# Kernel tuning notes

Hardware: AMD Instinct MI355X
Metric: run time of the kernel (lower is better)

Reference implementation:

```python
import jax, jax.numpy as jnp
import numpy as np

EMBED_DIM = 1024
HEADS = 16
D_HEAD = EMBED_DIM // HEADS
B, S = 2, 2048


def setup_inputs() -> dict:
    key = jax.random.key(0)
    ks = jax.random.split(key, 7)
    scale = 1.0 / np.sqrt(EMBED_DIM)
    inp = {
        "key": jax.random.normal(ks[0], (B, S, EMBED_DIM), dtype=jnp.float32),
        "query": jax.random.normal(ks[1], (B, S, EMBED_DIM), dtype=jnp.float32),
        "value": jax.random.normal(ks[2], (B, S, EMBED_DIM), dtype=jnp.float32),
        # causal mask, broadcastable to [B, H, Sq, Sk]
        "mask": jnp.tril(jnp.ones((S, S), dtype=bool))[None, None, :, :],
        # torch nn.Linear weights: [out_features, in_features], applied as x @ W.T
        "Wq": jax.random.normal(ks[3], (EMBED_DIM, EMBED_DIM), dtype=jnp.float32) * scale,
        "Wk": jax.random.normal(ks[4], (EMBED_DIM, EMBED_DIM), dtype=jnp.float32) * scale,
        "Wv": jax.random.normal(ks[5], (EMBED_DIM, EMBED_DIM), dtype=jnp.float32) * scale,
        "Wo": jax.random.normal(ks[6], (EMBED_DIM, EMBED_DIM), dtype=jnp.float32) * scale,
    }
    return inp


def reference(key, query, value, mask, Wq, Wk, Wv, Wo):
    b, sq, _ = query.shape
    sk = key.shape[1]
    # projections (torch Linear: x @ W.T), reshape to [B, H, S, Dh]
    q = (query @ Wq.T).reshape(b, sq, HEADS, D_HEAD).transpose(0, 2, 1, 3)
    k = (key @ Wk.T).reshape(b, sk, HEADS, D_HEAD).transpose(0, 2, 1, 3)
    v = (value @ Wv.T).reshape(b, sk, HEADS, D_HEAD).transpose(0, 2, 1, 3)
    # scaled dot-product scores [B, H, Sq, Sk]
    scores = jnp.einsum("bhqd,bhkd->bhqk", q, k) / jnp.sqrt(jnp.float32(D_HEAD))
    scores = jnp.where(mask, scores, jnp.float32(-1e9))
    attn = jax.nn.softmax(scores, axis=-1)
    # dropout p=0.0 -> identity
    out = jnp.einsum("bhqk,bhkd->bhqd", attn, v)  # [B, H, Sq, Dh]
    out = out.transpose(0, 2, 1, 3).reshape(b, sq, EMBED_DIM)
    return out @ Wo.T
```

## Files before the change

kernel.cpp:

```cpp
#include <hip/hip_runtime.h>
#include <stdint.h>


typedef unsigned short ushort_t;
typedef __attribute__((ext_vector_type(8))) __bf16 bf16x8;
typedef __attribute__((ext_vector_type(4))) float floatx4;

#define EMBED 1024
#define SEQ   2048
#define NH    16
#define DH    64
#define QK_SCALE 0.18033688011112042f

__device__ inline ushort_t f2b(float x) {
  unsigned u = __float_as_uint(x);
  u += 0x7FFFu + ((u >> 16) & 1u);
  return (ushort_t)(u >> 16);
}

__device__ inline unsigned pk2(float a, float b) {
  unsigned ua = __float_as_uint(a) + 0x8000u;
  unsigned ub = __float_as_uint(b) + 0x8000u;
  return __builtin_amdgcn_perm(ub, ua, 0x07060302u);
}

__device__ inline void gl_lds16(const ushort_t* g, ushort_t* l) {
  __builtin_amdgcn_global_load_lds(
      (const __attribute__((address_space(1))) unsigned int*)g,
      (__attribute__((address_space(3))) unsigned int*)l, 16, 0, 0);
}

struct CvtArgs {
  const float* src[16];
  ushort_t*    dst[16];
  float        scale[16];
};

__global__ __launch_bounds__(256) void cvt_kernel(CvtArgs a) {
  const int chunk = blockIdx.x >> 9;
  const int off = ((blockIdx.x & 511) << 11) + (threadIdx.x << 3);
  const float sc = a.scale[chunk];
  const float4* s = (const float4*)(a.src[chunk] + off);
  float4 f0 = s[0], f1 = s[1];
  union { ushort_t u[8]; uint4 v; } o;
  o.u[0] = f2b(f0.x * sc); o.u[1] = f2b(f0.y * sc);
  o.u[2] = f2b(f0.z * sc); o.u[3] = f2b(f0.w * sc);
  o.u[4] = f2b(f1.x * sc); o.u[5] = f2b(f1.y * sc);
  o.u[6] = f2b(f1.z * sc); o.u[7] = f2b(f1.w * sc);
  *(uint4*)(a.dst[chunk] + off) = o.v;
}

template <int NSUB>
__device__ inline void gemm_core(const ushort_t* __restrict__ A,
                                 const ushort_t* __restrict__ W,
                                 char* __restrict__ Cv, const int mode,
                                 const int K, const int ldc,
                                 const int m0, const int n0) {
  __shared__ ushort_t As[16 * 512];
  __shared__ ushort_t Bs[NSUB * 4 * 512];
  const int tid  = threadIdx.x;
  const int lane = tid & 63;
  const int wid  = tid >> 6;
  const int lm   = lane & 15;
  const int quad = lane >> 4;

  int grow[4], gcol[4];
#pragma unroll
  for (int i = 0; i < 4; ++i) {
    const int c = wid + 4 * i;
    grow[i] = (c >> 1) * 16 + lm;
    gcol[i] = (c & 1) * 32 + quad * 8;
  }

  floatx4 zero = {0.f, 0.f, 0.f, 0.f};
  floatx4 acc[4][NSUB];
#pragma unroll
  for (int i = 0; i < 4; ++i)
#pragma unroll
    for (int j = 0; j < NSUB; ++j) acc[i][j] = zero;

  const int tm = (wid >> 1) * 4;
  const int tn = (wid & 1) * NSUB;

  for (int k0 = 0; k0 < K; k0 += 64) {
    __syncthreads();
#pragma unroll
    for (int i = 0; i < 4; ++i)
      gl_lds16(A + (size_t)(m0 + grow[i]) * K + k0 + gcol[i], &As[(wid + 4 * i) * 512]);
#pragma unroll
    for (int i = 0; i < NSUB; ++i)
      gl_lds16(W + (size_t)(n0 + grow[i]) * K + k0 + gcol[i], &Bs[(wid + 4 * i) * 512]);
    __syncthreads();

#pragma unroll
    for (int ks = 0; ks < 2; ++ks) {
      bf16x8 a[4], b[NSUB];
#pragma unroll
      for (int i = 0; i < 4; ++i)
        a[i] = *(const bf16x8*)&As[((tm + i) * 2 + ks) * 512 + lane * 8];
#pragma unroll
      for (int j = 0; j < NSUB; ++j)
        b[j] = *(const bf16x8*)&Bs[((tn + j) * 2 + ks) * 512 + lane * 8];
#pragma unroll
      for (int i = 0; i < 4; ++i)
#pragma unroll
        for (int j = 0; j < NSUB; ++j)
          acc[i][j] = __builtin_amdgcn_mfma_f32_16x16x32_bf16(a[i], b[j], acc[i][j], 0, 0, 0);
    }
  }

#pragma unroll
  for (int i = 0; i < 4; ++i) {
    const int row = m0 + (wid >> 1) * 64 + i * 16 + quad * 4;
#pragma unroll
    for (int j = 0; j < NSUB; ++j) {
      const int col = n0 + (wid & 1) * (NSUB * 16) + j * 16 + lm;
      if (mode == 0) {
        ushort_t* C = (ushort_t*)Cv;
#pragma unroll
        for (int r = 0; r < 4; ++r)
          C[(size_t)(row + r) * ldc + col] = f2b(acc[i][j][r]);
      } else if (mode == 1) {
        float* C = (float*)Cv;
#pragma unroll
        for (int r = 0; r < 4; ++r)
          C[(size_t)(row + r) * ldc + col] = acc[i][j][r];
      } else {
        ushort_t* C = (ushort_t*)Cv;
        const int b = row >> 11, s = row & 2047;
        const int h = col >> 6, d = col & 63;
        union { ushort_t u[4]; uint2 v; } pk;
#pragma unroll
        for (int r = 0; r < 4; ++r) pk.u[r] = f2b(acc[i][j][r]);
        *(uint2*)&C[(size_t)((b * NH + h) * DH + d) * SEQ + s] = pk.v;
      }
    }
  }
}

struct QkvArgs {
  const ushort_t* A[3];
  const ushort_t* W[3];
  char*           C[3];
};

__global__ __launch_bounds__(256) void qkv_gemm(QkvArgs q) {
  const int z = blockIdx.z;
  gemm_core<4>(q.A[z], q.W[z], q.C[z], z == 2 ? 2 : 0, EMBED, EMBED,
               blockIdx.x * 128, blockIdx.y * 128);
}

__global__ __launch_bounds__(256) void o_gemm(const ushort_t* __restrict__ A,
                                              const ushort_t* __restrict__ W,
                                              float* __restrict__ C) {
  gemm_core<2>(A, W, (char*)C, 1, EMBED, EMBED, blockIdx.x * 128, blockIdx.y * 64);
}

__global__ __launch_bounds__(256) void attn_kernel(const ushort_t* __restrict__ Qp,
                                                   const ushort_t* __restrict__ Kp,
                                                   const ushort_t* __restrict__ VpT,
                                                   ushort_t* __restrict__ Ob) {
  __shared__ ushort_t Qs[8 * 512];
  __shared__ ushort_t Ks[8 * 512];
  __shared__ ushort_t VTs[8 * 512];
  __shared__ ushort_t Pw[4 * 1024];
  const int L = blockIdx.x;
  const int xcd = L & 7;
  const int idx = L >> 3;
  const int z = idx & 15;
  const int bh = (idx >> 4) * 8 + xcd;
  const int h = bh & (NH - 1), b = bh >> 4;
  const int tid = threadIdx.x, lane = tid & 63, wid = tid >> 6;
  const int lm = lane & 15, quad = lane >> 4;
  const size_t qkbase = ((size_t)b * SEQ) * EMBED + h * DH;
  const size_t vtbase = ((size_t)(b * NH + h)) * DH * SEQ;

  for (int phase = 0; phase < 2; ++phase) {
    const int qt = phase ? (31 - z) : z;

    __syncthreads();
#pragma unroll
    for (int ks = 0; ks < 2; ++ks)
      gl_lds16(Qp + qkbase + (size_t)(qt * 64 + wid * 16 + lm) * EMBED + ks * 32 + quad * 8,
               &Qs[(wid * 2 + ks) * 512]);
    __syncthreads();
    bf16x8 qf[2];
#pragma unroll
    for (int ks = 0; ks < 2; ++ks)
      qf[ks] = *(const bf16x8*)&Qs[(wid * 2 + ks) * 512 + lane * 8];

    float l_part = 0.f;
    floatx4 zero = {0.f, 0.f, 0.f, 0.f};
    floatx4 o_acc[4];
#pragma unroll
    for (int d = 0; d < 4; ++d) o_acc[d] = zero;

    for (int kt = 0; kt <= qt; ++kt) {
      __syncthreads();
#pragma unroll
      for (int u = 0; u < 2; ++u) {
        const int t = wid + u * 4, sub = t >> 1, half = t & 1;
        gl_lds16(Kp + qkbase + (size_t)(kt * 64 + sub * 16 + lm) * EMBED + half * 32 + quad * 8,
                 &Ks[t * 512]);
        gl_lds16(VpT + vtbase + (size_t)(sub * 16 + lm) * SEQ + kt * 64 + half * 32 + quad * 8,
                 &VTs[t * 512]);
      }
      __syncthreads();

      floatx4 s_acc[4];
#pragma unroll
      for (int i = 0; i < 4; ++i) s_acc[i] = zero;
#pragma unroll
      for (int ks = 0; ks < 2; ++ks)
#pragma unroll
        for (int i = 0; i < 4; ++i) {
          bf16x8 kf = *(const bf16x8*)&Ks[(i * 2 + ks) * 512 + lane * 8];
          s_acc[i] = __builtin_amdgcn_mfma_f32_16x16x32_bf16(kf, qf[ks], s_acc[i], 0, 0, 0);
        }

      float p[4][4];
#pragma unroll
      for (int i = 0; i < 4; ++i)
#pragma unroll
        for (int r = 0; r < 4; ++r)
          p[i][r] = __builtin_amdgcn_exp2f(s_acc[i][r]);
      if (kt == qt) {
#pragma unroll
        for (int i = 0; i < 4; ++i)
#pragma unroll
          for (int r = 0; r < 4; ++r)
            if (i * 16 + quad * 4 + r > wid * 16 + lm) p[i][r] = 0.f;
      }
#pragma unroll
      for (int i = 0; i < 4; ++i)
#pragma unroll
        for (int r = 0; r < 4; ++r) l_part += p[i][r];

      ushort_t* pwb = &Pw[wid * 1024];
#pragma unroll
      for (int i = 0; i < 4; ++i) {
        const int kkstep = i >> 1;
        const int quadB = ((i & 1) << 1) | (quad >> 1);
        uint2 pk;
        pk.x = pk2(p[i][0], p[i][1]);
        pk.y = pk2(p[i][2], p[i][3]);
        *(uint2*)&pwb[kkstep * 512 + (quadB * 16 + lm) * 8 + ((quad & 1) << 2)] = pk;
      }
      asm volatile("s_waitcnt lgkmcnt(0)" ::: "memory");

#pragma unroll
      for (int kkstep = 0; kkstep < 2; ++kkstep) {
        bf16x8 pf = *(const bf16x8*)&pwb[kkstep * 512 + lane * 8];
#pragma unroll
        for (int d = 0; d < 4; ++d) {
          bf16x8 vf = *(const bf16x8*)&VTs[(d * 2 + kkstep) * 512 + lane * 8];
          o_acc[d] = __builtin_amdgcn_mfma_f32_16x16x32_bf16(vf, pf, o_acc[d], 0, 0, 0);
        }
      }
    }

    float l = l_part;
    l += __shfl_xor(l, 16, 64);
    l += __shfl_xor(l, 32, 64);
    const float inv_l = 1.0f / l;

    const size_t orow = qkbase + (size_t)(qt * 64 + wid * 16 + lm) * EMBED;
#pragma unroll
    for (int d = 0; d < 4; ++d) {
      uint2 pk;
      pk.x = pk2(o_acc[d][0] * inv_l, o_acc[d][1] * inv_l);
      pk.y = pk2(o_acc[d][2] * inv_l, o_acc[d][3] * inv_l);
      *(uint2*)&Ob[orow + d * 16 + quad * 4] = pk;
    }
  }
}

extern "C" void kernel_launch(void* const* d_in, const int* in_sizes, int n_in,
                              void* d_out, int out_size, void* d_ws, size_t ws_size,
                              hipStream_t stream) {
  const float* key   = (const float*)d_in[0];
  const float* query = (const float*)d_in[1];
  const float* value = (const float*)d_in[2];
  const float* Wq = (const float*)d_in[4];
  const float* Wk = (const float*)d_in[5];
  const float* Wv = (const float*)d_in[6];
  const float* Wo = (const float*)d_in[7];

  char* ws = (char*)d_ws;
  const size_t MB = 1024 * 1024;
  ushort_t* Xk  = (ushort_t*)(ws + 0 * MB);
  ushort_t* Xq  = (ushort_t*)(ws + 8 * MB);
  ushort_t* Xv  = (ushort_t*)(ws + 16 * MB);
  ushort_t* Wqb = (ushort_t*)(ws + 24 * MB);
  ushort_t* Wkb = (ushort_t*)(ws + 26 * MB);
  ushort_t* Wvb = (ushort_t*)(ws + 28 * MB);
  ushort_t* Wob = (ushort_t*)(ws + 30 * MB);
  ushort_t* Qp  = (ushort_t*)(ws + 32 * MB);
  ushort_t* Kp  = (ushort_t*)(ws + 40 * MB);
  ushort_t* VpT = (ushort_t*)(ws + 48 * MB);
  ushort_t* Ob  = (ushort_t*)(ws + 56 * MB);

  CvtArgs ca;
  const size_t CE = 1048576;
  for (int c = 0; c < 16; ++c) ca.scale[c] = 1.0f;
  for (int c = 0; c < 4; ++c) { ca.src[c]     = key   + c * CE; ca.dst[c]     = Xk + c * CE; }
  for (int c = 0; c < 4; ++c) { ca.src[4 + c] = query + c * CE; ca.dst[4 + c] = Xq + c * CE; }
  for (int c = 0; c < 4; ++c) { ca.src[8 + c] = value + c * CE; ca.dst[8 + c] = Xv + c * CE; }
  ca.src[12] = Wq; ca.dst[12] = Wqb; ca.scale[12] = QK_SCALE;
  ca.src[13] = Wk; ca.dst[13] = Wkb;
  ca.src[14] = Wv; ca.dst[14] = Wvb;
  ca.src[15] = Wo; ca.dst[15] = Wob;
  cvt_kernel<<<8192, 256, 0, stream>>>(ca);

  QkvArgs qa;
  qa.A[0] = Xq; qa.W[0] = Wqb; qa.C[0] = (char*)Qp;
  qa.A[1] = Xk; qa.W[1] = Wkb; qa.C[1] = (char*)Kp;
  qa.A[2] = Xv; qa.W[2] = Wvb; qa.C[2] = (char*)VpT;
  qkv_gemm<<<dim3(32, 8, 3), 256, 0, stream>>>(qa);

  attn_kernel<<<512, 256, 0, stream>>>(Qp, Kp, VpT, Ob);

  o_gemm<<<dim3(32, 16), 256, 0, stream>>>(Ob, Wob, (float*)d_out);
}
```

Measured before the change: 256.4 us.

## Enlarge attention tiles to 128x128 and remap GEMM grids for XCD locality

After: 300.5 us. +17.2%, slower.

```diff
diff --git a/kernel.cpp b/kernel.cpp
--- a/kernel.cpp
+++ b/kernel.cpp
@@ -145,132 +145,151 @@
 };
 
 __global__ __launch_bounds__(256) void qkv_gemm(QkvArgs q) {
-  const int z = blockIdx.z;
+  const int L = blockIdx.x;
+  const int y = L & 7, t = L >> 3;
+  const int x = t & 31, z = t >> 5;
   gemm_core<4>(q.A[z], q.W[z], q.C[z], z == 2 ? 2 : 0, EMBED, EMBED,
-               blockIdx.x * 128, blockIdx.y * 128);
+               x * 128, y * 128);
 }
 
 __global__ __launch_bounds__(256) void o_gemm(const ushort_t* __restrict__ A,
                                               const ushort_t* __restrict__ W,
                                               float* __restrict__ C) {
-  gemm_core<2>(A, W, (char*)C, 1, EMBED, EMBED, blockIdx.x * 128, blockIdx.y * 64);
+  const int L = blockIdx.x;
+  gemm_core<4>(A, W, (char*)C, 1, EMBED, EMBED, (L >> 3) * 128, (L & 7) * 128);
 }
 
 __global__ __launch_bounds__(256) void attn_kernel(const ushort_t* __restrict__ Qp,
                                                    const ushort_t* __restrict__ Kp,
                                                    const ushort_t* __restrict__ VpT,
                                                    ushort_t* __restrict__ Ob) {
-  __shared__ ushort_t Qs[8 * 512];
-  __shared__ ushort_t Ks[8 * 512];
-  __shared__ ushort_t VTs[8 * 512];
-  __shared__ ushort_t Pw[4 * 1024];
+  __shared__ ushort_t Qs[16 * 512];
+  __shared__ ushort_t Ks[16 * 512];
+  __shared__ ushort_t VTs[16 * 512];
+  __shared__ ushort_t Pw[4 * 4096];
   const int L = blockIdx.x;
-  const int xcd = L & 7;
-  const int idx = L >> 3;
-  const int z = idx & 15;
-  const int bh = (idx >> 4) * 8 + xcd;
+  const int xcd = L & 7, t = L >> 3;
+  const int z = t & 7;
+  const int bh = (t >> 3) * 8 + xcd;
   const int h = bh & (NH - 1), b = bh >> 4;
   const int tid = threadIdx.x, lane = tid & 63, wid = tid >> 6;
   const int lm = lane & 15, quad = lane >> 4;
   const size_t qkbase = ((size_t)b * SEQ) * EMBED + h * DH;
   const size_t vtbase = ((size_t)(b * NH + h)) * DH * SEQ;
+  ushort_t* pwb = &Pw[wid * 4096];
 
   for (int phase = 0; phase < 2; ++phase) {
-    const int qt = phase ? (31 - z) : z;
-
-    __syncthreads();
-#pragma unroll
-    for (int ks = 0; ks < 2; ++ks)
-      gl_lds16(Qp + qkbase + (size_t)(qt * 64 + wid * 16 + lm) * EMBED + ks * 32 + quad * 8,
-               &Qs[(wid * 2 + ks) * 512]);
-    __syncthreads();
-    bf16x8 qf[2];
-#pragma unroll
-    for (int ks = 0; ks < 2; ++ks)
-      qf[ks] = *(const bf16x8*)&Qs[(wid * 2 + ks) * 512 + lane * 8];
-
-    float l_part = 0.f;
+    const int qb = phase ? (15 - z) : z;
+
+#pragma unroll
+    for (int u = 0; u < 4; ++u) {
+      const int c = wid * 4 + u;
+      gl_lds16(Qp + qkbase + (size_t)(qb * 128 + (c >> 1) * 16 + lm) * EMBED
+                   + (c & 1) * 32 + quad * 8,
+               &Qs[c * 512]);
+    }
+    asm volatile("s_waitcnt vmcnt(0)" ::: "memory");
+    bf16x8 qf[2][2];
+#pragma unroll
+    for (int qg = 0; qg < 2; ++qg)
+#pragma unroll
+      for (int ks = 0; ks < 2; ++ks)
+        qf[qg][ks] = *(const bf16x8*)&Qs[((wid * 2 + qg) * 2 + ks) * 512 + lane * 8];
+
+    float l_part[2] = {0.f, 0.f};
     floatx4 zero = {0.f, 0.f, 0.f, 0.f};
-    floatx4 o_acc[4];
-#pragma unroll
-    for (int d = 0; d < 4; ++d) o_acc[d] = zero;
-
-    for (int kt = 0; kt <= qt; ++kt) {
+    floatx4 o_acc[4][2];
+#pragma unroll
+    for (int d = 0; d < 4; ++d)
+#pragma unroll
+      for (int qg = 0; qg < 2; ++qg) o_acc[d][qg] = zero;
+
+    for (int kt = 0; kt <= qb; ++kt) {
       __syncthreads();
 #pragma unroll
-      for (int u = 0; u < 2; ++u) {
-        const int t = wid + u * 4, sub = t >> 1, half = t & 1;
-        gl_lds16(Kp + qkbase + (size_t)(kt * 64 + sub * 16 + lm) * EMBED + half * 32 + quad * 8,
-                 &Ks[t * 512]);
-        gl_lds16(VpT + vtbase + (size_t)(sub * 16 + lm) * SEQ + kt * 64 + half * 32 + quad * 8,
-                 &VTs[t * 512]);
+      for (int u = 0; u < 4; ++u) {
+        const int c = wid * 4 + u;
+        gl_lds16(Kp + qkbase + (size_t)(kt * 128 + (c >> 1) * 16 + lm) * EMBED
+                     + (c & 1) * 32 + quad * 8,
+                 &Ks[c * 512]);
+        gl_lds16(VpT + vtbase + (size_t)((c >> 2) * 16 + lm) * SEQ
+                     + kt * 128 + (c & 3) * 32 + quad * 8,
+                 &VTs[c * 512]);
       }
       __syncthreads();
 
-      floatx4 s_acc[4];
-#pragma unroll
-      for (int i = 0; i < 4; ++i) s_acc[i] = zero;
+      floatx4 s_acc[8][2];
+#pragma unroll
+      for (int i = 0; i < 8; ++i)
+#pragma unroll
+        for (int qg = 0; qg < 2; ++qg) s_acc[i][qg] = zero;
 #pragma unroll
       for (int ks = 0; ks < 2; ++ks)
 #pragma unroll
-        for (int i = 0; i < 4; ++i) {
+        for (int i = 0; i < 8; ++i) {
           bf16x8 kf = *(const bf16x8*)&Ks[(i * 2 + ks) * 512 + lane * 8];
-          s_acc[i] = __builtin_amdgcn_mfma_f32_16x16x32_bf16(kf, qf[ks], s_acc[i], 0, 0, 0);
+#pragma unroll
+          for (int qg = 0; qg < 2; ++qg)
+            s_acc[i][qg] = __builtin_amdgcn_mfma_f32_16x16x32_bf16(kf, qf[qg][ks], s_acc[i][qg], 0, 0, 0);
         }
 
-      float p[4][4];
-#pragma unroll
-      for (int i = 0; i < 4; ++i)
-#pragma unroll
-        for (int r = 0; r < 4; ++r)
-          p[i][r] = __builtin_amdgcn_exp2f(s_acc[i][r]);
-      if (kt == qt) {
-#pragma unroll
-        for (int i = 0; i < 4; ++i)
-#pragma unroll
-          for (int r = 0; r < 4; ++r)
-            if (i * 16 + quad * 4 + r > wid * 16 + lm) p[i][r] = 0.f;
-      }
-#pragma unroll
-      for (int i = 0; i < 4; ++i)
-#pragma unroll
-        for (int r = 0; r < 4; ++r) l_part += p[i][r];
-
-      ushort_t* pwb = &Pw[wid * 1024];
-#pragma unroll
-      for (int i = 0; i < 4; ++i) {
-        const int kkstep = i >> 1;
+      const bool diag = (kt == qb);
+#pragma unroll
+      for (int i = 0; i < 8; ++i) {
+        const int s = i >> 1;
         const int quadB = ((i & 1) << 1) | (quad >> 1);
+        const int kkl = i * 16 + quad * 4;
+#pragma unroll
+        for (int qg = 0; qg < 2; ++qg) {
+          float p[4];
+#pragma unroll
+          for (int r = 0; r < 4; ++r) p[r] = __builtin_amdgcn_exp2f(s_acc[i][qg][r]);
+          if (diag) {
+            const int ql = wid * 32 + qg * 16 + lm;
+#pragma unroll
+            for (int r = 0; r < 4; ++r)
+              if (kkl + r > ql) p[r] = 0.f;
+          }
+#pragma unroll
+          for (int r = 0; r < 4; ++r) l_part[qg] += p[r];
+          uint2 pk;
+          pk.x = pk2(p[0], p[1]);
+          pk.y = pk2(p[2], p[3]);
+          *(uint2*)&pwb[(qg * 4 + s) * 512 + (quadB * 16 + lm) * 8 + ((quad & 1) << 2)] = pk;
+        }
+      }
+      asm volatile("s_waitcnt lgkmcnt(0)" ::: "memory");
+
+#pragma unroll
+      for (int s = 0; s < 4; ++s) {
+        bf16x8 pf[2];
+#pragma unroll
+        for (int qg = 0; qg < 2; ++qg)
+          pf[qg] = *(const bf16x8*)&pwb[(qg * 4 + s) * 512 + lane * 8];
+#pragma unroll
+        for (int d = 0; d < 4; ++d) {
+          bf16x8 vf = *(const bf16x8*)&VTs[(d * 4 + s) * 512 + lane * 8];
+#pragma unroll
+          for (int qg = 0; qg < 2; ++qg)
+            o_acc[d][qg] = __builtin_amdgcn_mfma_f32_16x16x32_bf16(vf, pf[qg], o_acc[d][qg], 0, 0, 0);
+        }
+      }
+    }
+
+#pragma unroll
+    for (int qg = 0; qg < 2; ++qg) {
+      float l = l_part[qg];
+      l += __shfl_xor(l, 16, 64);
+      l += __shfl_xor(l, 32, 64);
+      const float inv_l = 1.0f / l;
+      const size_t orow = qkbase + (size_t)(qb * 128 + wid * 32 + qg * 16 + lm) * EMBED;
+#pragma unroll
+      for (int d = 0; d < 4; ++d) {
         uint2 pk;
-        pk.x = pk2(p[i][0], p[i][1]);
-        pk.y = pk2(p[i][2], p[i][3]);
-        *(uint2*)&pwb[kkstep * 512 + (quadB * 16 + lm) * 8 + ((quad & 1) << 2)] = pk;
-      }
-      asm volatile("s_waitcnt lgkmcnt(0)" ::: "memory");
-
-#pragma unroll
-      for (int kkstep = 0; kkstep < 2; ++kkstep) {
-        bf16x8 pf = *(const bf16x8*)&pwb[kkstep * 512 + lane * 8];
-#pragma unroll
-        for (int d = 0; d < 4; ++d) {
-          bf16x8 vf = *(const bf16x8*)&VTs[(d * 2 + kkstep) * 512 + lane * 8];
-          o_acc[d] = __builtin_amdgcn_mfma_f32_16x16x32_bf16(vf, pf, o_acc[d], 0, 0, 0);
-        }
-      }
-    }
-
-    float l = l_part;
-    l += __shfl_xor(l, 16, 64);
-    l += __shfl_xor(l, 32, 64);
-    const float inv_l = 1.0f / l;
-
-    const size_t orow = qkbase + (size_t)(qt * 64 + wid * 16 + lm) * EMBED;
-#pragma unroll
-    for (int d = 0; d < 4; ++d) {
-      uint2 pk;
-      pk.x = pk2(o_acc[d][0] * inv_l, o_acc[d][1] * inv_l);
-      pk.y = pk2(o_acc[d][2] * inv_l, o_acc[d][3] * inv_l);
-      *(uint2*)&Ob[orow + d * 16 + quad * 4] = pk;
+        pk.x = pk2(o_acc[d][qg][0] * inv_l, o_acc[d][qg][1] * inv_l);
+        pk.y = pk2(o_acc[d][qg][2] * inv_l, o_acc[d][qg][3] * inv_l);
+        *(uint2*)&Ob[orow + d * 16 + quad * 4] = pk;
+      }
     }
   }
 }
@@ -316,9 +335,9 @@
   qa.A[0] = Xq; qa.W[0] = Wqb; qa.C[0] = (char*)Qp;
   qa.A[1] = Xk; qa.W[1] = Wkb; qa.C[1] = (char*)Kp;
   qa.A[2] = Xv; qa.W[2] = Wvb; qa.C[2] = (char*)VpT;
-  qkv_gemm<<<dim3(32, 8, 3), 256, 0, stream>>>(qa);
-
-  attn_kernel<<<512, 256, 0, stream>>>(Qp, Kp, VpT, Ob);
-
-  o_gemm<<<dim3(32, 16), 256, 0, stream>>>(Ob, Wob, (float*)d_out);
-}
+  qkv_gemm<<<768, 256, 0, stream>>>(qa);
+
+  attn_kernel<<<256, 256, 0, stream>>>(Qp, Kp, VpT, Ob);
+
+  o_gemm<<<256, 256, 0, stream>>>(Ob, Wob, (float*)d_out);
+}
```
